# Performance work log

Measured on AMD Instinct MI355X. Metric: run time of the kernel, lower is better.

## Reference

```python
import jax, jax.numpy as jnp
import numpy as np

B, S, D, H, L, W, O = 4, 1024, 512, 8, 6, 64, 300
DH = D // H          # head dim = 64
R = 2 * W + 3        # rel_proj output dim = 131
EPS = 1e-6


def setup_inputs() -> dict:
    key = jax.random.key(0)
    ks = jax.random.split(key, 12)
    sc = 0.02
    x = jax.random.normal(ks[0], (B, S, D), jnp.float32)
    inp = {
        "x": x,
        "ln1_g": jnp.ones((L, D), jnp.float32),
        "ln1_b": jnp.zeros((L, D), jnp.float32),
        "qkv_w": jax.random.normal(ks[1], (L, D, 3 * D), jnp.float32) * sc,
        "qkv_b": jnp.zeros((L, 3 * D), jnp.float32),
        "rel_w": jax.random.normal(ks[2], (DH, R), jnp.float32) * sc,
        "rel_b": jnp.zeros((R,), jnp.float32),
        "ln2_g": jnp.ones((L, D), jnp.float32),
        "ln2_b": jnp.zeros((L, D), jnp.float32),
        "mlp_w1": jax.random.normal(ks[3], (L, D, 4 * D), jnp.float32) * sc,
        "mlp_b1": jnp.zeros((L, 4 * D), jnp.float32),
        "mlp_w2": jax.random.normal(ks[4], (L, 4 * D, D), jnp.float32) * sc,
        "mlp_b2": jnp.zeros((L, D), jnp.float32),
        "normf_g": jnp.ones((D,), jnp.float32),
        "normf_b": jnp.zeros((D,), jnp.float32),
        "head_w": jax.random.normal(ks[5], (D, O), jnp.float32) * sc,
        "head_b": jnp.zeros((O,), jnp.float32),
        "mask": jax.random.randint(ks[6], (B, O), 0, 2, jnp.int32),
    }
    return inp


def _layernorm(x, g, b):
    m = jnp.mean(x, axis=-1, keepdims=True)
    v = jnp.mean(jnp.square(x - m), axis=-1, keepdims=True)
    return (x - m) * jax.lax.rsqrt(v + EPS) * g + b


def _forward(x, ln1_g, ln1_b, qkv_w, qkv_b, rel_w, rel_b, ln2_g, ln2_b,
             mlp_w1, mlp_b1, mlp_w2, mlp_b2, normf_g, normf_b, head_w, head_b, mask):
    b, s, d = x.shape
    # clamped relative offsets, shifted to [0, 2W]; shape [s, s]
    ar = jnp.arange(s)
    offsets = jnp.clip(ar[None, :] - ar[:, None], -W, W) + W
    off_bh = jnp.broadcast_to(offsets[None, None], (b, H, s, s))
    scale = 1.0 / np.sqrt(D / H)  # = 1/sqrt(dh)

    def block(xc, lp):
        (l1g, l1b, qw, qb, l2g, l2b, w1, b1, w2, b2) = lp
        h = _layernorm(xc, l1g, l1b)
        qkv = (h @ qw + qb).reshape(b, s, H, 3 * DH)
        q, k, v = jnp.split(qkv, 3, axis=-1)            # [b,s,h,dh] each
        q = q.transpose(0, 2, 1, 3)                     # [b,h,s,dh]
        k = k.transpose(0, 2, 1, 3)
        v = v.transpose(0, 2, 1, 3)
        content = jnp.einsum('bhik,bhjk->bhij', q, k) * scale
        pos = q @ rel_w + rel_b                          # [b,h,s,R]
        pos_scores = jnp.take_along_axis(pos, off_bh, axis=-1)  # [b,h,s,s]
        attn = jax.nn.softmax(content + pos_scores, axis=-1)
        out = jnp.einsum('bhij,bhjk->bhik', attn, v)     # [b,h,s,dh]
        xc = xc + out.transpose(0, 2, 1, 3).reshape(b, s, d)
        h2 = _layernorm(xc, l2g, l2b)
        m = jax.nn.gelu(h2 @ w1 + b1, approximate=False) @ w2 + b2
        return xc + m, None

    layer_params = (ln1_g, ln1_b, qkv_w, qkv_b, ln2_g, ln2_b,
                    mlp_w1, mlp_b1, mlp_w2, mlp_b2)
    x, _ = jax.lax.scan(block, x, layer_params)
    x = _layernorm(x, normf_g, normf_b)[:, 0, :]         # CLS token
    logits = x @ head_w + head_b                          # [b, O]
    return jnp.where(mask == 0, -jnp.inf, logits)


def reference(x, ln1_g, ln1_b, qkv_w, qkv_b, rel_w, rel_b, ln2_g, ln2_b,
              mlp_w1, mlp_b1, mlp_w2, mlp_b2, normf_g, normf_b, head_w, head_b, mask):
    return _forward(x, ln1_g, ln1_b, qkv_w, qkv_b, rel_w, rel_b, ln2_g, ln2_b,
                    mlp_w1, mlp_b1, mlp_w2, mlp_b2, normf_g, normf_b, head_w, head_b, mask)
```

## Files before the change

kernel.cpp:

```cpp
#include <hip/hip_runtime.h>
#include <math.h>

#define B_  4
#define S_  1024
#define D_  512
#define H_  8
#define L_  6
#define W_  64
#define O_  300
#define DH_ 64
#define R_  131
#define R2_ 132

#define HSTRIDE_   262144
#define PARTSTR_   2097152

typedef __attribute__((ext_vector_type(8))) short bf16x8;
typedef __attribute__((ext_vector_type(4))) float f32x4;

#define SWZ(r) ((((r) ^ ((r) >> 3)) & 7) << 4)

__device__ __forceinline__ float gelu_f(float x) {
    return 0.5f * x * (1.0f + erff(x * 0.70710678118654752f));
}

__device__ __forceinline__ unsigned short f2bf(float f) {
    union { float f; unsigned u; } c; c.f = f;
    unsigned u = c.u;
    unsigned r = (u + 0x7fffu + ((u >> 16) & 1u)) >> 16;
    return (unsigned short)r;
}
__device__ __forceinline__ float bf2f(unsigned short u) {
    union { unsigned u; float f; } c; c.u = ((unsigned)u) << 16; return c.f;
}

__device__ __forceinline__ void gload_lds16(const void* g, void* l) {
    __builtin_amdgcn_global_load_lds(
        (const __attribute__((address_space(1))) unsigned int*)g,
        (__attribute__((address_space(3))) unsigned int*)l, 16, 0, 0);
}

__global__ __launch_bounds__(256) void ln_kernel(
    const float* __restrict__ x, const float* __restrict__ g,
    const float* __restrict__ b, unsigned short* __restrict__ y, int rows)
{
    int wave = threadIdx.x >> 6;
    int lane = threadIdx.x & 63;
    int row0 = blockIdx.x * 8 + wave * 2;
    if (row0 >= rows) return;
    const float* xr0 = x + (size_t)row0 * D_;
    const float* xr1 = xr0 + D_;
    float4 a0v = *(const float4*)(xr0 + lane * 4);
    float4 a1v = *(const float4*)(xr0 + 256 + lane * 4);
    float4 b0v = *(const float4*)(xr1 + lane * 4);
    float4 b1v = *(const float4*)(xr1 + 256 + lane * 4);

    float sa = a0v.x + a0v.y + a0v.z + a0v.w + a1v.x + a1v.y + a1v.z + a1v.w;
    float sb = b0v.x + b0v.y + b0v.z + b0v.w + b1v.x + b1v.y + b1v.z + b1v.w;
    #pragma unroll
    for (int off = 32; off >= 1; off >>= 1) {
        sa += __shfl_xor(sa, off);
        sb += __shfl_xor(sb, off);
    }
    float ma = sa * (1.0f / 512.0f), mb = sb * (1.0f / 512.0f);

    float a0 = a0v.x - ma, a1 = a0v.y - ma, a2 = a0v.z - ma, a3 = a0v.w - ma;
    float a4 = a1v.x - ma, a5 = a1v.y - ma, a6 = a1v.z - ma, a7 = a1v.w - ma;
    float c0 = b0v.x - mb, c1 = b0v.y - mb, c2 = b0v.z - mb, c3 = b0v.w - mb;
    float c4 = b1v.x - mb, c5 = b1v.y - mb, c6 = b1v.z - mb, c7 = b1v.w - mb;
    float va = a0*a0 + a1*a1 + a2*a2 + a3*a3 + a4*a4 + a5*a5 + a6*a6 + a7*a7;
    float vb = c0*c0 + c1*c1 + c2*c2 + c3*c3 + c4*c4 + c5*c5 + c6*c6 + c7*c7;
    #pragma unroll
    for (int off = 32; off >= 1; off >>= 1) {
        va += __shfl_xor(va, off);
        vb += __shfl_xor(vb, off);
    }
    float ra = rsqrtf(va * (1.0f / 512.0f) + 1e-6f);
    float rb = rsqrtf(vb * (1.0f / 512.0f) + 1e-6f);

    float4 g0 = *(const float4*)(g + lane * 4);
    float4 g1 = *(const float4*)(g + 256 + lane * 4);
    float4 bb0 = *(const float4*)(b + lane * 4);
    float4 bb1 = *(const float4*)(b + 256 + lane * 4);

    unsigned short* yr0 = y + (size_t)row0 * D_;
    unsigned short* yr1 = yr0 + D_;
    ushort4 p0 = {f2bf(a0 * ra * g0.x + bb0.x), f2bf(a1 * ra * g0.y + bb0.y),
                  f2bf(a2 * ra * g0.z + bb0.z), f2bf(a3 * ra * g0.w + bb0.w)};
    ushort4 p1 = {f2bf(a4 * ra * g1.x + bb1.x), f2bf(a5 * ra * g1.y + bb1.y),
                  f2bf(a6 * ra * g1.z + bb1.z), f2bf(a7 * ra * g1.w + bb1.w)};
    ushort4 q0 = {f2bf(c0 * rb * g0.x + bb0.x), f2bf(c1 * rb * g0.y + bb0.y),
                  f2bf(c2 * rb * g0.z + bb0.z), f2bf(c3 * rb * g0.w + bb0.w)};
    ushort4 q1 = {f2bf(c4 * rb * g1.x + bb1.x), f2bf(c5 * rb * g1.y + bb1.y),
                  f2bf(c6 * rb * g1.z + bb1.z), f2bf(c7 * rb * g1.w + bb1.w)};
    *(ushort4*)(yr0 + lane * 4)       = p0;
    *(ushort4*)(yr0 + 256 + lane * 4) = p1;
    *(ushort4*)(yr1 + lane * 4)       = q0;
    *(ushort4*)(yr1 + 256 + lane * 4) = q1;
}

__global__ __launch_bounds__(256) void tconv_kernel(
    const float* __restrict__ in, unsigned short* __restrict__ out, int K, int N)
{
    __shared__ float t[32][33];
    int tx = threadIdx.x & 31, ty = threadIdx.x >> 5;
    int n0 = blockIdx.x * 32, k0 = blockIdx.y * 32;
    #pragma unroll
    for (int j = 0; j < 4; ++j)
        t[ty + 8*j][tx] = in[(size_t)(k0 + ty + 8*j) * N + n0 + tx];
    __syncthreads();
    #pragma unroll
    for (int j = 0; j < 4; ++j)
        out[(size_t)(n0 + ty + 8*j) * K + k0 + tx] = f2bf(t[tx][ty + 8*j]);
}

__global__ __launch_bounds__(256) void relw_prep(
    const float* __restrict__ rel_w, unsigned short* __restrict__ relwT)
{
    for (int i = threadIdx.x; i < 144 * 64; i += 256) {
        int r = i >> 6, c = i & 63;
        relwT[i] = (r < R_) ? f2bf(rel_w[(size_t)c * R_ + r]) : (unsigned short)0;
    }
}

__global__ __launch_bounds__(256) void prep_all(
    const float* __restrict__ qkv_w, const float* __restrict__ mlp_w1,
    const float* __restrict__ mlp_w2, const float* __restrict__ rel_w,
    unsigned short* __restrict__ wTq_all, unsigned short* __restrict__ wT1_all,
    unsigned short* __restrict__ wT2_all, unsigned short* __restrict__ relwT)
{
    int bid = blockIdx.x;
    int tid = threadIdx.x;
    if (bid >= 4224) {
        for (int i = tid; i < 144 * 64; i += 256) {
            int r = i >> 6, c = i & 63;
            relwT[i] = (r < R_) ? f2bf(rel_w[(size_t)c * R_ + r]) : (unsigned short)0;
        }
        return;
    }
    int l = bid / 704, rr = bid - l * 704;
    const float* in; unsigned short* out; int K, N, bk, bn2;
    if (rr < 192) {
        in = qkv_w + (size_t)l * 512 * 1536; out = wTq_all + (size_t)l * 1536 * 512;
        K = 512; N = 1536; bk = rr / 24; bn2 = rr % 24;
    } else if (rr < 448) {
        int r2 = rr - 192;
        in = mlp_w1 + (size_t)l * 512 * 2048; out = wT1_all + (size_t)l * 2048 * 512;
        K = 512; N = 2048; bk = r2 / 32; bn2 = r2 % 32;
    } else {
        int r2 = rr - 448;
        in = mlp_w2 + (size_t)l * 2048 * 512; out = wT2_all + (size_t)l * 512 * 2048;
        K = 2048; N = 512; bk = r2 / 8; bn2 = r2 % 8;
    }
    int k0 = bk * 64, n0 = bn2 * 64;
    __shared__ unsigned short st[64][72];
    #pragma unroll
    for (int p = 0; p < 4; ++p) {
        int c = p * 256 + tid;
        int kr = c >> 4, n4 = (c & 15) * 4;
        float4 v = *(const float4*)(in + (size_t)(k0 + kr) * N + n0 + n4);
        int s0 = ((n4 >> 2) & 7) << 3;
        int kc = kr ^ s0;
        st[n4 + 0][kc] = f2bf(v.x);
        st[n4 + 1][kc] = f2bf(v.y);
        st[n4 + 2][kc] = f2bf(v.z);
        st[n4 + 3][kc] = f2bf(v.w);
    }
    __syncthreads();
    #pragma unroll
    for (int p = 0; p < 2; ++p) {
        int c = p * 256 + tid;
        int nr = c >> 3, k8 = (c & 7) * 8;
        int kc8 = k8 ^ (((nr >> 2) & 7) << 3);
        bf16x8 val = *(const bf16x8*)(&st[nr][kc8]);
        *(bf16x8*)(out + (size_t)(n0 + nr) * K + k0 + k8) = val;
    }
}

template<int ACT, int OBF, int OUT3, int BM, int BN, int WM, int WN, int BK>
__global__ __launch_bounds__(256) void mfma_gemm(
    const unsigned short* __restrict__ A, const unsigned short* __restrict__ BT,
    const float* __restrict__ bias, const float* __restrict__ resid,
    void* __restrict__ Cout, int M, int N, int K)
{
    static_assert(WM * WN == 4, "4 waves");
    static_assert(!OUT3 || (OBF && BN == 64), "OUT3 needs bf16 out, BN=64");
    constexpr int MFR = BM / WM / 16;
    constexpr int NFR = BN / WN / 16;
    constexpr int TPR = BK / 8;
    constexpr int RPP = 256 / TPR;
    constexpr int ACH = BM / RPP, BCH = BN / RPP;
    constexpr int LOADS = ACH + BCH;
    constexpr int KK = BK / 32;
    __shared__ __align__(16) unsigned short smem[2 * (BM + BN) * BK];
    unsigned short* As = smem;
    unsigned short* Bs = smem + 2 * BM * BK;
    int tid  = threadIdx.x;
    int lane = tid & 63;
    int l15 = lane & 15, l4 = lane >> 4;
    int wid  = tid >> 6;
    int wave_m = (wid / WN) * (BM / WM);
    int wave_n = (wid % WN) * (BN / WN);

    int nwg = gridDim.x * gridDim.y;
    int bid0 = blockIdx.y * gridDim.x + blockIdx.x;
    int bid = (bid0 & 7) * (nwg >> 3) + (bid0 >> 3);
    int bm = (bid / gridDim.x) * BM, bn = (bid % gridDim.x) * BN;

    const f32x4 z4 = {0.f, 0.f, 0.f, 0.f};
    f32x4 acc[MFR][NFR];
    #pragma unroll
    for (int m = 0; m < MFR; ++m)
        #pragma unroll
        for (int n = 0; n < NFR; ++n) acc[m][n] = z4;

    int arow = tid / TPR;
    int acol8 = ((tid % TPR) ^ (arow & (TPR - 1))) * 8;
    const unsigned short* Ab = A  + (size_t)(bm + arow) * K + acol8;
    const unsigned short* Bb = BT + (size_t)(bn + arow) * K + acol8;
    unsigned short* Adst = As + tid * 8;
    unsigned short* Bdst = Bs + tid * 8;

    int swzA = l15 & (TPR - 1);
    const unsigned short* Afrag = As + (size_t)(wave_m + l15) * BK;
    const unsigned short* Bfrag = Bs + (size_t)(wave_n + l15) * BK;

    const int NT = K / BK;

    auto STAGE = [&](int buf, int k0) {
        #pragma unroll
        for (int ch = 0; ch < ACH; ++ch)
            gload_lds16(Ab + (size_t)ch * RPP * K + k0, Adst + buf * BM * BK + ch * RPP * BK);
        #pragma unroll
        for (int ch = 0; ch < BCH; ++ch)
            gload_lds16(Bb + (size_t)ch * RPP * K + k0, Bdst + buf * BN * BK + ch * RPP * BK);
    };

    STAGE(0, 0);
    STAGE(1, BK);

    int off8[KK];
    #pragma unroll
    for (int kk = 0; kk < KK; ++kk) off8[kk] = ((l4 + 4 * kk) ^ swzA) * 8;

    for (int t = 0; t < NT; ++t) {
        int cur = t & 1;
        if (t + 1 < NT) {
            if constexpr (LOADS == 8) asm volatile("s_waitcnt vmcnt(8)" ::: "memory");
            else if constexpr (LOADS == 6) asm volatile("s_waitcnt vmcnt(6)" ::: "memory");
            else if constexpr (LOADS == 4) asm volatile("s_waitcnt vmcnt(4)" ::: "memory");
            else asm volatile("s_waitcnt vmcnt(0)" ::: "memory");
        } else {
            asm volatile("s_waitcnt vmcnt(0)" ::: "memory");
        }
        __builtin_amdgcn_s_barrier();
        asm volatile("" ::: "memory");

        const unsigned short* Af = Afrag + cur * BM * BK;
        const unsigned short* Bf = Bfrag + cur * BN * BK;
        bf16x8 af[KK][MFR], bfr[KK][NFR];
        #pragma unroll
        for (int kk = 0; kk < KK; ++kk) {
            #pragma unroll
            for (int m = 0; m < MFR; ++m) af[kk][m]  = *(const bf16x8*)(Af + m * 16 * BK + off8[kk]);
            #pragma unroll
            for (int n = 0; n < NFR; ++n) bfr[kk][n] = *(const bf16x8*)(Bf + n * 16 * BK + off8[kk]);
        }
        asm volatile("s_waitcnt lgkmcnt(0)" ::: "memory");
        __builtin_amdgcn_sched_barrier(0);
        __builtin_amdgcn_s_barrier();
        asm volatile("" ::: "memory");

        if (t + 2 < NT) STAGE(cur, (t + 2) * BK);

        __builtin_amdgcn_s_setprio(1);
        #pragma unroll
        for (int kk = 0; kk < KK; ++kk)
            #pragma unroll
            for (int m = 0; m < MFR; ++m)
                #pragma unroll
                for (int n = 0; n < NFR; ++n)
                    acc[m][n] = __builtin_amdgcn_mfma_f32_16x16x32_bf16(af[kk][m], bfr[kk][n], acc[m][n], 0, 0, 0);
        __builtin_amdgcn_s_setprio(0);
    }

    if constexpr (OBF) {
        constexpr int STR = BN + 8;
        unsigned short* st = smem;
        #pragma unroll
        for (int m = 0; m < MFR; ++m) {
            #pragma unroll
            for (int n = 0; n < NFR; ++n) {
                int lc = wave_n + n * 16 + l15;
                float bv = bias[bn + lc];
                #pragma unroll
                for (int q = 0; q < 4; ++q) {
                    int lr = wave_m + m * 16 + l4 * 4 + q;
                    float v = acc[m][n][q] + bv;
                    if (ACT == 1) v = gelu_f(v);
                    st[lr * STR + lc] = f2bf(v);
                }
            }
        }
        __syncthreads();
        constexpr int PASS = BM * BN / (256 * 8);
        if constexpr (OUT3) {
            int bnt = bn >> 6;
            int part = bnt % 3, hh = bnt / 3;
            unsigned short* dst = (unsigned short*)Cout + (size_t)part * PARTSTR_ + (size_t)hh * HSTRIDE_;
            #pragma unroll
            for (int p = 0; p < PASS; ++p) {
                int flat = (p * 256 + tid) * 8;
                int row = flat >> 6, col = flat & 63;
                bf16x8 val = *(const bf16x8*)(st + row * STR + col);
                *(bf16x8*)(dst + (size_t)(bm + row) * 64 + col) = val;
            }
        } else {
            #pragma unroll
            for (int p = 0; p < PASS; ++p) {
                int flat = (p * 256 + tid) * 8;
                int row = flat / BN, col = flat % BN;
                bf16x8 val = *(const bf16x8*)(st + row * STR + col);
                *(bf16x8*)((unsigned short*)Cout + (size_t)(bm + row) * N + bn + col) = val;
            }
        }
    } else {
        constexpr int STR = BN + 4;
        float* st = (float*)smem;
        #pragma unroll
        for (int m = 0; m < MFR; ++m) {
            #pragma unroll
            for (int n = 0; n < NFR; ++n) {
                int lc = wave_n + n * 16 + l15;
                float bv = bias[bn + lc];
                #pragma unroll
                for (int q = 0; q < 4; ++q) {
                    int lr = wave_m + m * 16 + l4 * 4 + q;
                    float v = acc[m][n][q] + bv;
                    if (ACT == 1) v = gelu_f(v);
                    st[lr * STR + lc] = v;
                }
            }
        }
        __syncthreads();
        constexpr int PASS = BM * BN / (256 * 4);
        #pragma unroll
        for (int p = 0; p < PASS; ++p) {
            int flat = (p * 256 + tid) * 4;
            int row = flat / BN, col = flat % BN;
            float4 val = *(const float4*)(st + row * STR + col);
            if (resid) {
                float4 rr = *(const float4*)(resid + (size_t)(bm + row) * N + bn + col);
                val.x += rr.x; val.y += rr.y; val.z += rr.z; val.w += rr.w;
            }
            *(float4*)((float*)Cout + (size_t)(bm + row) * N + bn + col) = val;
        }
    }
}

__global__ __launch_bounds__(512, 2) void attn_mfma(
    const unsigned short* __restrict__ qs,
    const unsigned short* __restrict__ relwT,
    const float* __restrict__ rel_b,
    float* __restrict__ xres)
{
    __shared__ __align__(16) unsigned char shm[49664];
    unsigned char* Klds  = shm;
    unsigned char* Vtlds = shm + 16384;
    unsigned short* pos16 = (unsigned short*)(shm + 32768);
    float* mergeO  = (float*)shm;
    float* mergeML = (float*)(shm + 17408);

    int tid = threadIdx.x, lane = tid & 63, w = tid >> 6;
    int l15 = lane & 15, l4 = lane >> 4;
    int wq = w & 3;
    int g  = w >> 2;

    int lin = blockIdx.x;
    int xcd = lin & 7, j = lin >> 3;
    int gidx = xcd * 4 + (j >> 4);
    int b = gidx >> 3, h = gidx & 7;
    int it0 = (j & 15) * 64;

    const unsigned short* Qb = qs + (size_t)h * HSTRIDE_;
    const unsigned short* Kb = Qb + PARTSTR_;
    const unsigned short* Vb = Qb + 2 * PARTSTR_;
    int gs0 = b * S_;

    const float LOG2E = 1.4426950408889634f;
    const float SC = 0.125f * LOG2E;
    const float THR = 11.5441f;

    bf16x8 qa[2];
    {
        const unsigned short* qp = Qb + (size_t)(gs0 + it0 + wq * 16 + l15) * 64 + l4 * 8;
        qa[0] = *(const bf16x8*)(qp);
        qa[1] = *(const bf16x8*)(qp + 32);
    }

    if (g == 0) {
        #pragma unroll
        for (int n = 0; n < 9; ++n) {
            f32x4 pacc = {0.f, 0.f, 0.f, 0.f};
            #pragma unroll
            for (int ks = 0; ks < 2; ++ks) {
                bf16x8 bv = *(const bf16x8*)(relwT + (size_t)(16 * n + l15) * 64 + ks * 32 + l4 * 8);
                pacc = __builtin_amdgcn_mfma_f32_16x16x32_bf16(qa[ks], bv, pacc, 0, 0, 0);
            }
            int c = 16 * n + l15;
            if (c < R_) {
                float rb = rel_b[c];
                #pragma unroll
                for (int q = 0; q < 4; ++q)
                    pos16[(wq * 16 + l4 * 4 + q) * R2_ + c] = f2bf((pacc[q] + rb) * LOG2E);
            }
        }
    }
    __syncthreads();

    int rloc = wq * 16 + l15;
    int i_glob = it0 + rloc;
    float p_lo = bf2f(pos16[rloc * R2_ + 0]);
    float p_hi = bf2f(pos16[rloc * R2_ + 128]);

    int rf = tid >> 2, seg = tid & 3;
    int gk = rf >> 6, rr = rf & 63;
    const unsigned short* kbase = Kb + (size_t)(gs0 + gk * 512 + rr) * 64 + seg * 16;
    int kbyt = gk * 8192 + ((rr * 128 + seg * 32) ^ SWZ(rr));
    int pf = tid >> 3, seg8 = tid & 7;
    int gv = pf >> 5, pp = pf & 31;
    const unsigned short* vbase = Vb + (size_t)(gs0 + gv * 512 + 2 * pp) * 64 + seg8 * 8;
    bf16x8 kr0, kr1, vr0, vr1;
    kr0 = *(const bf16x8*)(kbase);
    kr1 = *(const bf16x8*)(kbase + 8);
    vr0 = *(const bf16x8*)(vbase);
    vr1 = *(const bf16x8*)(vbase + 64);

    const f32x4 z4 = {0.f, 0.f, 0.f, 0.f};
    f32x4 oacc[4];
    #pragma unroll
    for (int n = 0; n < 4; ++n) oacc[n] = z4;
    float mrun_s = -INFINITY, lrun_s = 0.f;
    int wmin = it0 + wq * 16;
    unsigned char* Kw = Klds + g * 8192;
    unsigned char* Vw = Vtlds + g * 8192;

    int idx_lo = (l15 + 32 * (l4 & 1)) * 4;
    int idx_hi = idx_lo + 64;
    bool hi_n = (l4 >> 1) != 0;

    for (int t = 0; t < 8; ++t) {
        int jt0 = g * 512 + t * 64;
        __syncthreads();
        *(bf16x8*)(Klds + kbyt) = kr0;
        *(bf16x8*)(Klds + (kbyt ^ 16)) = kr1;
        #pragma unroll
        for (int i = 0; i < 8; ++i) {
            int dh = seg8 * 8 + i;
            unsigned v01 = (unsigned)(unsigned short)vr0[i] | ((unsigned)(unsigned short)vr1[i] << 16);
            *(unsigned*)(Vtlds + gv * 8192 + ((dh * 128 + pp * 4) ^ SWZ(dh))) = v01;
        }
        __syncthreads();
        if (t < 7) {
            const unsigned short* kp = kbase + (size_t)(t + 1) * 4096;
            kr0 = *(const bf16x8*)(kp);
            kr1 = *(const bf16x8*)(kp + 8);
            const unsigned short* vp = vbase + (size_t)(t + 1) * 4096;
            vr0 = *(const bf16x8*)(vp);
            vr1 = *(const bf16x8*)(vp + 64);
        }

        f32x4 ssw[4];
        #pragma unroll
        for (int n = 0; n < 4; ++n) ssw[n] = z4;
        __builtin_amdgcn_s_setprio(1);
        #pragma unroll
        for (int n = 0; n < 4; ++n) {
            int kvr = 16 * n + l15;
            #pragma unroll
            for (int ks = 0; ks < 2; ++ks) {
                bf16x8 ak = *(const bf16x8*)(Kw + ((kvr * 128 + ks * 64 + l4 * 16) ^ SWZ(kvr)));
                ssw[n] = __builtin_amdgcn_mfma_f32_16x16x32_bf16(ak, qa[ks], ssw[n], 0, 0, 0);
            }
        }
        __builtin_amdgcn_s_setprio(0);

        float sv[4][4];
        bool left  = (jt0 + 63 < wmin - 64);
        bool right = (jt0 > wmin + 15 + 64);
        if (left || right) {
            float pc = left ? p_lo : p_hi;
            #pragma unroll
            for (int n = 0; n < 4; ++n)
                #pragma unroll
                for (int r = 0; r < 4; ++r) sv[n][r] = fmaf(ssw[n][r], SC, pc);
        } else {
            #pragma unroll
            for (int n = 0; n < 4; ++n)
                #pragma unroll
                for (int r = 0; r < 4; ++r) {
                    int jj = jt0 + 16 * n + l4 * 4 + r;
                    int off = jj - i_glob;
                    off = off < -64 ? -64 : (off > 64 ? 64 : off);
                    sv[n][r] = fmaf(ssw[n][r], SC, bf2f(pos16[rloc * R2_ + off + 64]));
                }
        }

        float a0 = fmaxf(fmaxf(sv[0][0], sv[0][1]), fmaxf(sv[0][2], sv[0][3]));
        float a1 = fmaxf(fmaxf(sv[1][0], sv[1][1]), fmaxf(sv[1][2], sv[1][3]));
        float a2 = fmaxf(fmaxf(sv[2][0], sv[2][1]), fmaxf(sv[2][2], sv[2][3]));
        float a3 = fmaxf(fmaxf(sv[3][0], sv[3][1]), fmaxf(sv[3][2], sv[3][3]));
        float mx = fmaxf(fmaxf(a0, a1), fmaxf(a2, a3));
        mx = fmaxf(mx, __shfl_xor(mx, 16));
        mx = fmaxf(mx, __shfl_xor(mx, 32));
        if (!__all(mx - mrun_s <= THR)) {
            float mnew = fmaxf(mrun_s, mx);
            float al = exp2f(mrun_s - mnew);
            mrun_s = mnew;
            lrun_s *= al;
            float alv0 = __shfl(al, l4 * 4 + 0);
            float alv1 = __shfl(al, l4 * 4 + 1);
            float alv2 = __shfl(al, l4 * 4 + 2);
            float alv3 = __shfl(al, l4 * 4 + 3);
            #pragma unroll
            for (int n = 0; n < 4; ++n) {
                oacc[n][0] *= alv0; oacc[n][1] *= alv1;
                oacc[n][2] *= alv2; oacc[n][3] *= alv3;
            }
        }
        float rs = 0.f;
        #pragma unroll
        for (int n = 0; n < 4; ++n)
            #pragma unroll
            for (int r = 0; r < 4; ++r) {
                float p = exp2f(sv[n][r] - mrun_s);
                sv[n][r] = p;
                rs += p;
            }
        rs += __shfl_xor(rs, 16);
        rs += __shfl_xor(rs, 32);
        lrun_s += rs;

        unsigned pkk[4][2];
        #pragma unroll
        for (int n = 0; n < 4; ++n) {
            asm("v_cvt_pk_bf16_f32 %0, %1, %2" : "=v"(pkk[n][0]) : "v"(sv[n][0]), "v"(sv[n][1]));
            asm("v_cvt_pk_bf16_f32 %0, %1, %2" : "=v"(pkk[n][1]) : "v"(sv[n][2]), "v"(sv[n][3]));
        }
        bf16x8 pa[2];
        #pragma unroll
        for (int ks = 0; ks < 2; ++ks) {
            unsigned wrd[4];
            #pragma unroll
            for (int ww = 0; ww < 4; ++ww) {
                int srcidx = (ww >> 1) ? idx_hi : idx_lo;
                unsigned vlo = (unsigned)__builtin_amdgcn_ds_bpermute(srcidx, (int)pkk[2 * ks + 0][ww & 1]);
                unsigned vhi = (unsigned)__builtin_amdgcn_ds_bpermute(srcidx, (int)pkk[2 * ks + 1][ww & 1]);
                wrd[ww] = hi_n ? vhi : vlo;
            }
            union { unsigned u[4]; bf16x8 v; } cvt;
            cvt.u[0] = wrd[0]; cvt.u[1] = wrd[1]; cvt.u[2] = wrd[2]; cvt.u[3] = wrd[3];
            pa[ks] = cvt.v;
        }

        __builtin_amdgcn_s_setprio(1);
        #pragma unroll
        for (int n = 0; n < 4; ++n) {
            int dh = 16 * n + l15;
            #pragma unroll
            for (int ks = 0; ks < 2; ++ks) {
                bf16x8 bv = *(const bf16x8*)(Vw + ((dh * 128 + ks * 64 + l4 * 16) ^ SWZ(dh)));
                oacc[n] = __builtin_amdgcn_mfma_f32_16x16x32_bf16(pa[ks], bv, oacc[n], 0, 0, 0);
            }
        }
        __builtin_amdgcn_s_setprio(0);
    }

    __syncthreads();
    if (g == 1) {
        #pragma unroll
        for (int n = 0; n < 4; ++n)
            #pragma unroll
            for (int r = 0; r < 4; ++r)
                mergeO[(wq * 16 + l4 * 4 + r) * 68 + 16 * n + l15] = oacc[n][r];
        if (lane < 16) {
            mergeML[rloc * 2 + 0] = mrun_s;
            mergeML[rloc * 2 + 1] = lrun_s;
        }
    }
    __syncthreads();
    if (g == 0) {
        float mb = mergeML[rloc * 2 + 0];
        float lb = mergeML[rloc * 2 + 1];
        float M  = fmaxf(mrun_s, mb);
        float fa = exp2f(mrun_s - M);
        float fb = exp2f(mb - M);
        float inv = 1.0f / (lrun_s * fa + lb * fb);
        float A_s = fa * inv, B_s = fb * inv;
        float Av[4], Bv[4];
        #pragma unroll
        for (int r = 0; r < 4; ++r) {
            Av[r] = __shfl(A_s, l4 * 4 + r);
            Bv[r] = __shfl(B_s, l4 * 4 + r);
        }
        #pragma unroll
        for (int r = 0; r < 4; ++r) {
            int row = wq * 16 + l4 * 4 + r;
            float* xp = xres + (size_t)(gs0 + it0 + row) * D_ + h * DH_;
            #pragma unroll
            for (int n = 0; n < 4; ++n)
                xp[16 * n + l15] += oacc[n][r] * Av[r] + mergeO[row * 68 + 16 * n + l15] * Bv[r];
        }
    }
}

__global__ __launch_bounds__(256) void head_kernel(
    const float* __restrict__ xc, const float* __restrict__ gf,
    const float* __restrict__ bfp, const float* __restrict__ hw,
    const float* __restrict__ hbias, const int* __restrict__ mask,
    float* __restrict__ out)
{
    __shared__ float a[4][512];
    __shared__ float part[4][64][4];
    int tid = threadIdx.x;
    int wv = tid >> 6, lane = tid & 63;
    {
        const float* xr = xc + (size_t)wv * S_ * D_;
        float4 v0 = *(const float4*)(xr + lane * 4);
        float4 v1 = *(const float4*)(xr + 256 + lane * 4);
        float s = v0.x + v0.y + v0.z + v0.w + v1.x + v1.y + v1.z + v1.w;
        #pragma unroll
        for (int off = 32; off >= 1; off >>= 1) s += __shfl_xor(s, off);
        float mean = s * (1.0f / 512.0f);
        float c0 = v0.x - mean, c1 = v0.y - mean, c2 = v0.z - mean, c3 = v0.w - mean;
        float c4 = v1.x - mean, c5 = v1.y - mean, c6 = v1.z - mean, c7 = v1.w - mean;
        float vs = c0*c0 + c1*c1 + c2*c2 + c3*c3 + c4*c4 + c5*c5 + c6*c6 + c7*c7;
        #pragma unroll
        for (int off = 32; off >= 1; off >>= 1) vs += __shfl_xor(vs, off);
        float rstd = rsqrtf(vs * (1.0f / 512.0f) + 1e-6f);
        float4 g0 = *(const float4*)(gf + lane * 4);
        float4 g1 = *(const float4*)(gf + 256 + lane * 4);
        float4 b0 = *(const float4*)(bfp + lane * 4);
        float4 b1 = *(const float4*)(bfp + 256 + lane * 4);
        a[wv][lane * 4 + 0] = c0 * rstd * g0.x + b0.x;
        a[wv][lane * 4 + 1] = c1 * rstd * g0.y + b0.y;
        a[wv][lane * 4 + 2] = c2 * rstd * g0.z + b0.z;
        a[wv][lane * 4 + 3] = c3 * rstd * g0.w + b0.w;
        a[wv][256 + lane * 4 + 0] = c4 * rstd * g1.x + b1.x;
        a[wv][256 + lane * 4 + 1] = c5 * rstd * g1.y + b1.y;
        a[wv][256 + lane * 4 + 2] = c6 * rstd * g1.z + b1.z;
        a[wv][256 + lane * 4 + 3] = c7 * rstd * g1.w + b1.w;
    }
    __syncthreads();

    int cl = tid & 63;
    int c  = blockIdx.x * 64 + cl;
    int ks = tid >> 6;
    float ac[4] = {0.f, 0.f, 0.f, 0.f};
    if (c < O_) {
        const float* wp = hw + (size_t)(ks * 128) * O_ + c;
        #pragma unroll 8
        for (int k = 0; k < 128; ++k) {
            float wvv = wp[(size_t)k * O_];
            int kk = ks * 128 + k;
            ac[0] = fmaf(a[0][kk], wvv, ac[0]);
            ac[1] = fmaf(a[1][kk], wvv, ac[1]);
            ac[2] = fmaf(a[2][kk], wvv, ac[2]);
            ac[3] = fmaf(a[3][kk], wvv, ac[3]);
        }
    }
    #pragma unroll
    for (int bb = 0; bb < 4; ++bb) part[ks][cl][bb] = ac[bb];
    __syncthreads();
    if (ks == 0 && c < O_) {
        float hbv = hbias[c];
        #pragma unroll
        for (int bb = 0; bb < 4; ++bb) {
            float v = part[0][cl][bb] + part[1][cl][bb] + part[2][cl][bb] + part[3][cl][bb] + hbv;
            out[bb * O_ + c] = (mask[bb * O_ + c] == 0) ? -1e30f : v;
        }
    }
}

extern "C" void kernel_launch(void* const* d_in, const int* in_sizes, int n_in,
                              void* d_out, int out_size, void* d_ws, size_t ws_size,
                              hipStream_t stream) {
    const float* x      = (const float*)d_in[0];
    const float* ln1_g  = (const float*)d_in[1];
    const float* ln1_b  = (const float*)d_in[2];
    const float* qkv_w  = (const float*)d_in[3];
    const float* qkv_b  = (const float*)d_in[4];
    const float* rel_w  = (const float*)d_in[5];
    const float* rel_b  = (const float*)d_in[6];
    const float* ln2_g  = (const float*)d_in[7];
    const float* ln2_b  = (const float*)d_in[8];
    const float* mlp_w1 = (const float*)d_in[9];
    const float* mlp_b1 = (const float*)d_in[10];
    const float* mlp_w2 = (const float*)d_in[11];
    const float* mlp_b2 = (const float*)d_in[12];
    const float* normf_g = (const float*)d_in[13];
    const float* normf_b = (const float*)d_in[14];
    const float* head_w  = (const float*)d_in[15];
    const float* head_b  = (const float*)d_in[16];
    const int*   mask    = (const int*)d_in[17];
    float* out = (float*)d_out;
    float* ws  = (float*)d_ws;

    const int NR = B_ * S_;
    dim3 blk(256);

    float* x_cur = ws;
    float* reg2  = ws + 2097152;
    unsigned short* qkvs = (unsigned short*)reg2;
    unsigned short* midb = (unsigned short*)reg2;

    hipMemcpyAsync(x_cur, x, (size_t)NR * D_ * sizeof(float),
                   hipMemcpyDeviceToDevice, stream);

    bool hoist = ws_size >= (size_t)15995392 * 4;

    if (hoist) {
        unsigned short* hb      = (unsigned short*)(ws + 6291456);
        unsigned short* wTq_all = (unsigned short*)(ws + 7340032);
        unsigned short* wT1_all = (unsigned short*)(ws + 9699328);
        unsigned short* wT2_all = (unsigned short*)(ws + 12845056);
        unsigned short* relwT   = (unsigned short*)(ws + 15990784);

        prep_all<<<4225, blk, 0, stream>>>(qkv_w, mlp_w1, mlp_w2, rel_w,
                                           wTq_all, wT1_all, wT2_all, relwT);

        for (int l = 0; l < L_; ++l) {
            ln_kernel<<<NR / 8, blk, 0, stream>>>(x_cur, ln1_g + l * D_, ln1_b + l * D_, hb, NR);
            mfma_gemm<0, 1, 1, 128, 64, 4, 1, 64><<<dim3(24, 32), blk, 0, stream>>>(
                hb, wTq_all + (size_t)l * 1536 * 512, qkv_b + (size_t)l * 3 * D_,
                nullptr, qkvs, NR, 3 * D_, D_);
            attn_mfma<<<dim3(512), dim3(512), 0, stream>>>(qkvs, relwT, rel_b, x_cur);
            ln_kernel<<<NR / 8, blk, 0, stream>>>(x_cur, ln2_g + l * D_, ln2_b + l * D_, hb, NR);
            mfma_gemm<1, 1, 0, 128, 128, 2, 2, 64><<<dim3(16, 32), blk, 0, stream>>>(
                hb, wT1_all + (size_t)l * 2048 * 512, mlp_b1 + (size_t)l * 4 * D_,
                nullptr, midb, NR, 4 * D_, D_);
            mfma_gemm<0, 0, 0, 64, 64, 2, 2, 128><<<dim3(8, 64), blk, 0, stream>>>(
                midb, wT2_all + (size_t)l * 512 * 2048, mlp_b2 + (size_t)l * D_,
                x_cur, x_cur, NR, D_, 4 * D_);
        }
        head_kernel<<<dim3(5), blk, 0, stream>>>(x_cur, normf_g, normf_b,
                                                 head_w, head_b, mask, out);
    } else {
        float* wregs = ws + 6291456;
        unsigned short* hb    = (unsigned short*)wregs;
        unsigned short* wTq   = (unsigned short*)(wregs + 1048576);
        unsigned short* wT1   = (unsigned short*)(wregs + 1441792);
        unsigned short* wT2   = (unsigned short*)(wregs + 1966080);
        unsigned short* relwT = (unsigned short*)(ws + 10616832);

        relw_prep<<<1, blk, 0, stream>>>(rel_w, relwT);
        for (int l = 0; l < L_; ++l) {
            ln_kernel<<<NR / 8, blk, 0, stream>>>(x_cur, ln1_g + l * D_, ln1_b + l * D_, hb, NR);
            tconv_kernel<<<dim3(48, 16), blk, 0, stream>>>(
                qkv_w + (size_t)l * D_ * 3 * D_, wTq, D_, 3 * D_);
            mfma_gemm<0, 1, 1, 128, 64, 4, 1, 64><<<dim3(24, 32), blk, 0, stream>>>(
                hb, wTq, qkv_b + (size_t)l * 3 * D_, nullptr, qkvs, NR, 3 * D_, D_);
            attn_mfma<<<dim3(512), dim3(512), 0, stream>>>(qkvs, relwT, rel_b, x_cur);
            ln_kernel<<<NR / 8, blk, 0, stream>>>(x_cur, ln2_g + l * D_, ln2_b + l * D_, hb, NR);
            tconv_kernel<<<dim3(64, 16), blk, 0, stream>>>(
                mlp_w1 + (size_t)l * D_ * 4 * D_, wT1, D_, 4 * D_);
            mfma_gemm<1, 1, 0, 128, 128, 2, 2, 64><<<dim3(16, 32), blk, 0, stream>>>(
                hb, wT1, mlp_b1 + (size_t)l * 4 * D_, nullptr, midb, NR, 4 * D_, D_);
            tconv_kernel<<<dim3(16, 64), blk, 0, stream>>>(
                mlp_w2 + (size_t)l * 4 * D_ * D_, wT2, 4 * D_, D_);
            mfma_gemm<0, 0, 0, 64, 64, 2, 2, 128><<<dim3(8, 64), blk, 0, stream>>>(
                midb, wT2, mlp_b2 + (size_t)l * D_, x_cur, x_cur, NR, D_, 4 * D_);
        }
        head_kernel<<<dim3(5), blk, 0, stream>>>(x_cur, normf_g, normf_b,
                                                 head_w, head_b, mask, out);
    }
}
```

Measured before the change: 576.8 us.

## Load K fragments directly from global and double-buffer V in LDS

The attention kernel stops staging K through shared memory. Each wave now reads its K MFMA operands straight from global memory into registers. The transposed V tile is double-buffered in LDS, with the next tile written during the current iteration, so each loop step needs one barrier instead of two. The aim is to cut LDS traffic and barrier stalls, at the cost of redundant K global/L2 reads across the four waves of a group and K loads that are issued just before use with little latency hiding.

```diff
diff --git a/kernel.cpp b/kernel.cpp
--- a/kernel.cpp
+++ b/kernel.cpp
@@ -365,8 +365,7 @@
     float* __restrict__ xres)
 {
     __shared__ __align__(16) unsigned char shm[49664];
-    unsigned char* Klds  = shm;
-    unsigned char* Vtlds = shm + 16384;
+    unsigned char* Vtlds = shm;
     unsigned short* pos16 = (unsigned short*)(shm + 32768);
     float* mergeO  = (float*)shm;
     float* mergeML = (float*)(shm + 17408);
@@ -423,18 +422,14 @@
     float p_lo = bf2f(pos16[rloc * R2_ + 0]);
     float p_hi = bf2f(pos16[rloc * R2_ + 128]);
 
-    int rf = tid >> 2, seg = tid & 3;
-    int gk = rf >> 6, rr = rf & 63;
-    const unsigned short* kbase = Kb + (size_t)(gs0 + gk * 512 + rr) * 64 + seg * 16;
-    int kbyt = gk * 8192 + ((rr * 128 + seg * 32) ^ SWZ(rr));
     int pf = tid >> 3, seg8 = tid & 7;
     int gv = pf >> 5, pp = pf & 31;
     const unsigned short* vbase = Vb + (size_t)(gs0 + gv * 512 + 2 * pp) * 64 + seg8 * 8;
-    bf16x8 kr0, kr1, vr0, vr1;
-    kr0 = *(const bf16x8*)(kbase);
-    kr1 = *(const bf16x8*)(kbase + 8);
+    bf16x8 vr0, vr1;
     vr0 = *(const bf16x8*)(vbase);
     vr1 = *(const bf16x8*)(vbase + 64);
+
+    const unsigned short* kwbase = Kb + (size_t)(gs0 + g * 512 + l15) * 64 + l4 * 8;
 
     const f32x4 z4 = {0.f, 0.f, 0.f, 0.f};
     f32x4 oacc[4];
@@ -442,32 +437,44 @@
     for (int n = 0; n < 4; ++n) oacc[n] = z4;
     float mrun_s = -INFINITY, lrun_s = 0.f;
     int wmin = it0 + wq * 16;
-    unsigned char* Kw = Klds + g * 8192;
-    unsigned char* Vw = Vtlds + g * 8192;
 
     int idx_lo = (l15 + 32 * (l4 & 1)) * 4;
     int idx_hi = idx_lo + 64;
     bool hi_n = (l4 >> 1) != 0;
 
+    #pragma unroll
+    for (int i = 0; i < 8; ++i) {
+        int dh = seg8 * 8 + i;
+        unsigned v01 = (unsigned)(unsigned short)vr0[i] | ((unsigned)(unsigned short)vr1[i] << 16);
+        *(unsigned*)(Vtlds + gv * 8192 + ((dh * 128 + pp * 4) ^ SWZ(dh))) = v01;
+    }
+    vr0 = *(const bf16x8*)(vbase + 4096);
+    vr1 = *(const bf16x8*)(vbase + 4096 + 64);
+    __syncthreads();
+
     for (int t = 0; t < 8; ++t) {
+        int cur = t & 1;
         int jt0 = g * 512 + t * 64;
-        __syncthreads();
-        *(bf16x8*)(Klds + kbyt) = kr0;
-        *(bf16x8*)(Klds + (kbyt ^ 16)) = kr1;
-        #pragma unroll
-        for (int i = 0; i < 8; ++i) {
-            int dh = seg8 * 8 + i;
-            unsigned v01 = (unsigned)(unsigned short)vr0[i] | ((unsigned)(unsigned short)vr1[i] << 16);
-            *(unsigned*)(Vtlds + gv * 8192 + ((dh * 128 + pp * 4) ^ SWZ(dh))) = v01;
-        }
-        __syncthreads();
+        unsigned char* Vw = Vtlds + cur * 16384 + g * 8192;
+
+        bf16x8 ka[4][2];
+        #pragma unroll
+        for (int n = 0; n < 4; ++n)
+            #pragma unroll
+            for (int ks = 0; ks < 2; ++ks)
+                ka[n][ks] = *(const bf16x8*)(kwbase + (size_t)t * 4096 + n * 1024 + ks * 32);
+
         if (t < 7) {
-            const unsigned short* kp = kbase + (size_t)(t + 1) * 4096;
-            kr0 = *(const bf16x8*)(kp);
-            kr1 = *(const bf16x8*)(kp + 8);
-            const unsigned short* vp = vbase + (size_t)(t + 1) * 4096;
-            vr0 = *(const bf16x8*)(vp);
-            vr1 = *(const bf16x8*)(vp + 64);
+            #pragma unroll
+            for (int i = 0; i < 8; ++i) {
+                int dh = seg8 * 8 + i;
+                unsigned v01 = (unsigned)(unsigned short)vr0[i] | ((unsigned)(unsigned short)vr1[i] << 16);
+                *(unsigned*)(Vtlds + (cur ^ 1) * 16384 + gv * 8192 + ((dh * 128 + pp * 4) ^ SWZ(dh))) = v01;
+            }
+            if (t + 2 < 8) {
+                vr0 = *(const bf16x8*)(vbase + (size_t)(t + 2) * 4096);
+                vr1 = *(const bf16x8*)(vbase + (size_t)(t + 2) * 4096 + 64);
+            }
         }
 
         f32x4 ssw[4];
@@ -475,14 +482,10 @@
         for (int n = 0; n < 4; ++n) ssw[n] = z4;
         __builtin_amdgcn_s_setprio(1);
         #pragma unroll
-        for (int n = 0; n < 4; ++n) {
-            int kvr = 16 * n + l15;
-            #pragma unroll
-            for (int ks = 0; ks < 2; ++ks) {
-                bf16x8 ak = *(const bf16x8*)(Kw + ((kvr * 128 + ks * 64 + l4 * 16) ^ SWZ(kvr)));
-                ssw[n] = __builtin_amdgcn_mfma_f32_16x16x32_bf16(ak, qa[ks], ssw[n], 0, 0, 0);
-            }
-        }
+        for (int n = 0; n < 4; ++n)
+            #pragma unroll
+            for (int ks = 0; ks < 2; ++ks)
+                ssw[n] = __builtin_amdgcn_mfma_f32_16x16x32_bf16(ka[n][ks], qa[ks], ssw[n], 0, 0, 0);
         __builtin_amdgcn_s_setprio(0);
 
         float sv[4][4];
@@ -574,9 +577,10 @@
             }
         }
         __builtin_amdgcn_s_setprio(0);
-    }
-
-    __syncthreads();
+
+        __syncthreads();
+    }
+
     if (g == 1) {
         #pragma unroll
         for (int n = 0; n < 4; ++n)
```

New measurement: 631.1 us. 1.09x slower.
